# Performance work log

Measured on AMD Instinct MI355X. Metric: run time of the kernel, lower is better.

## Reference

```python
import jax, jax.numpy as jnp
import numpy as np
import math

HEAD = 4

def _neighbors3x3(t):
    # t: [b, g, d, h, w] -> [b, g, d, 9, h, w], zero-padded 3x3 neighborhoods
    b, g, d, h, w = t.shape
    tp = jnp.pad(t, ((0, 0), (0, 0), (0, 0), (1, 1), (1, 1)))
    # torch.nn.Unfold(kernel_size=3) ordering: kernel positions row-major (dy, dx)
    patches = [tp[:, :, :, dy:dy + h, dx:dx + w] for dy in range(3) for dx in range(3)]
    return jnp.stack(patches, axis=3)


def setup_inputs() -> dict:
    key = jax.random.key(0)
    k1, k2 = jax.random.split(key)
    x = jax.random.normal(k1, (8, 128, 96, 96), dtype=jnp.float32)
    # 1x1 conv weight, no bias: [out=3*out_features, in=in_features]
    W_trans = jax.random.normal(k2, (384, 128), dtype=jnp.float32) * 0.05
    return {"x": x, "W_trans": W_trans}


def reference(x, W_trans):
    b, cin, h, w = x.shape
    # 1x1 conv == channel GEMM
    t = jnp.einsum('bchw,oc->bohw', x, W_trans)  # [b, 3*C, h, w]
    q, k, v = jnp.split(t, 3, axis=1)            # each [b, C, h, w]
    C = q.shape[1]
    d = C // HEAD
    q = q.reshape(b, HEAD, d, h, w)
    k = k.reshape(b, HEAD, d, h, w)
    v = v.reshape(b, HEAD, d, h, w)
    kn = _neighbors3x3(k)  # [b, g, d, 9, h, w]
    vn = _neighbors3x3(v)  # [b, g, d, 9, h, w]
    # att[b,g,n,h,w] = <q[b,g,:,h,w], kn[b,g,:,n,h,w]> / sqrt(d)
    att = jnp.einsum('bgdhw,bgdnhw->bgnhw', q, kn) / math.sqrt(d)
    att = jax.nn.softmax(att, axis=2)
    # dropout p=0.4 is identity in eval mode
    out = jnp.einsum('bgnhw,bgdnhw->bgdhw', att, vn)  # [b, g, d, h, w]
    return out.reshape(b, C, h, w)
```

## Files before the change

### kernel.cpp

```cpp
#include <hip/hip_runtime.h>

#define NB     8
#define CIN    128
#define HEADS  4
#define DHEAD  32
#define HDIM   96
#define WDIM   96
#define HW     9216
#define TP     64

typedef __bf16 bf16x8 __attribute__((ext_vector_type(8)));
typedef float  f32x4  __attribute__((ext_vector_type(4)));

__device__ __forceinline__ unsigned f2bf(float f) {
  unsigned u = __float_as_uint(f);
  return (u + 0x7fffu + ((u >> 16) & 1u)) >> 16;
}
__device__ __forceinline__ unsigned pack2(float a, float b) {
  return f2bf(a) | (f2bf(b) << 16);
}
__device__ __forceinline__ float bflo(unsigned u) { return __uint_as_float(u << 16); }
__device__ __forceinline__ float bfhi(unsigned u) { return __uint_as_float(u & 0xffff0000u); }

__global__ __launch_bounds__(256) void wpack_kernel(const float* __restrict__ W,
                                                    uint4* __restrict__ Wf) {
  const int u = blockIdx.x * 256 + threadIdx.x;
  const int lane = u & 63, kb = (u >> 6) & 3, ot = u >> 8;
  const int o = ot * 16 + (lane & 15);
  const int c0 = kb * 32 + (lane >> 4) * 8;
  const float4* w = (const float4*)(W + (size_t)o * CIN + c0);
  float4 w0 = w[0], w1 = w[1];
  uint4 r;
  r.x = pack2(w0.x, w0.y); r.y = pack2(w0.z, w0.w);
  r.z = pack2(w1.x, w1.y); r.w = pack2(w1.z, w1.w);
  Wf[u] = r;
}

__global__ __launch_bounds__(256) void qkv_kernel(const float* __restrict__ x,
                                                  const uint4* __restrict__ Wf,
                                                  unsigned short* __restrict__ qkvb) {
  __shared__ uint4 xs[16 * 64];
  const int b  = blockIdx.y;
  const int p0 = blockIdx.x * TP;
  const int t  = threadIdx.x;

  {
    const int p = t & 63, cg_hi = t >> 6;
    const int pt = p >> 4, n = p & 15;
    const float* xb = x + (size_t)b * CIN * HW + p0 + p;
#pragma unroll
    for (int i = 0; i < 4; ++i) {
      const int cg = i * 4 + cg_hi;
      const int c0 = cg * 8;
      const int kb = cg >> 2, q = cg & 3;
      float f[8];
#pragma unroll
      for (int j = 0; j < 8; ++j) f[j] = xb[(size_t)(c0 + j) * HW];
      uint4 r;
      r.x = pack2(f[0], f[1]); r.y = pack2(f[2], f[3]);
      r.z = pack2(f[4], f[5]); r.w = pack2(f[6], f[7]);
      xs[(pt * 4 + kb) * 64 + q * 16 + n] = r;
    }
  }
  __syncthreads();

  const int wv = t >> 6, lane = t & 63;
  const int colp = lane & 15, quad = lane >> 4;
#pragma unroll 1
  for (int it = 0; it < 6; ++it) {
    const int ot = wv * 6 + it;
    bf16x8 afrag[4];
#pragma unroll
    for (int kb = 0; kb < 4; ++kb) {
      uint4 tmp = Wf[(ot * 4 + kb) * 64 + lane];
      afrag[kb] = *(bf16x8*)&tmp;
    }
    const int o0 = ot * 16 + quad * 4;
    const int which = o0 >> 7, g = (o0 & 127) >> 5, d0 = o0 & 31;
    unsigned short* dst = qkvb
        + (((size_t)(which * NB + b) * HEADS + g) * HW) * DHEAD + d0;
#pragma unroll
    for (int pt = 0; pt < 4; ++pt) {
      f32x4 acc = {0.f, 0.f, 0.f, 0.f};
#pragma unroll
      for (int kb = 0; kb < 4; ++kb) {
        bf16x8 bfrag = *(bf16x8*)&xs[(pt * 4 + kb) * 64 + lane];
        acc = __builtin_amdgcn_mfma_f32_16x16x32_bf16(afrag[kb], bfrag, acc, 0, 0, 0);
      }
      const int pp = p0 + pt * 16 + colp;
      uint2 st;
      st.x = pack2(acc[0], acc[1]);
      st.y = pack2(acc[2], acc[3]);
      *(uint2*)(dst + (size_t)pp * DHEAD) = st;
    }
  }
}

__global__ __launch_bounds__(256) void attn_kernel(const unsigned short* __restrict__ qkvb,
                                                   float* __restrict__ out) {
  const int bg = blockIdx.z;
  const int h  = blockIdx.y * 8 + threadIdx.y;
  const int w  = blockIdx.x * 32 + threadIdx.x;
  const int b  = bg >> 2, g = bg & 3;

  const size_t plane = (size_t)HW * DHEAD;
  const uint4* Qb = (const uint4*)(qkvb + (size_t)bg * plane);
  const uint4* Kb = (const uint4*)(qkvb + (size_t)(32 + bg) * plane);
  const uint4* Vb = (const uint4*)(qkvb + (size_t)(64 + bg) * plane);
  const int p = h * WDIM + w;

  float q[32];
#pragma unroll
  for (int i = 0; i < 4; ++i) {
    uint4 u = Qb[p * 4 + i];
    q[i * 8 + 0] = bflo(u.x); q[i * 8 + 1] = bfhi(u.x);
    q[i * 8 + 2] = bflo(u.y); q[i * 8 + 3] = bfhi(u.y);
    q[i * 8 + 4] = bflo(u.z); q[i * 8 + 5] = bfhi(u.z);
    q[i * 8 + 6] = bflo(u.w); q[i * 8 + 7] = bfhi(u.w);
  }

  float att[9];
#pragma unroll
  for (int nn = 0; nn < 9; ++nn) {
    const int dy = nn / 3 - 1, dx = nn % 3 - 1;
    const int hh = h + dy, ww = w + dx;
    float dot = 0.0f;
    if (hh >= 0 && hh < HDIM && ww >= 0 && ww < WDIM) {
      const int pn = hh * WDIM + ww;
#pragma unroll
      for (int i = 0; i < 4; ++i) {
        uint4 u = Kb[pn * 4 + i];
        dot = fmaf(q[i * 8 + 0], bflo(u.x), dot);
        dot = fmaf(q[i * 8 + 1], bfhi(u.x), dot);
        dot = fmaf(q[i * 8 + 2], bflo(u.y), dot);
        dot = fmaf(q[i * 8 + 3], bfhi(u.y), dot);
        dot = fmaf(q[i * 8 + 4], bflo(u.z), dot);
        dot = fmaf(q[i * 8 + 5], bfhi(u.z), dot);
        dot = fmaf(q[i * 8 + 6], bflo(u.w), dot);
        dot = fmaf(q[i * 8 + 7], bfhi(u.w), dot);
      }
      dot *= 0.17677669529663687f;
    }
    att[nn] = dot;
  }

  float m = att[0];
#pragma unroll
  for (int nn = 1; nn < 9; ++nn) m = fmaxf(m, att[nn]);
  float s = 0.0f;
#pragma unroll
  for (int nn = 0; nn < 9; ++nn) { att[nn] = __expf(att[nn] - m); s += att[nn]; }
  const float inv = 1.0f / s;

  float acc[32];
#pragma unroll
  for (int i = 0; i < 32; ++i) acc[i] = 0.0f;
#pragma unroll
  for (int nn = 0; nn < 9; ++nn) {
    const int dy = nn / 3 - 1, dx = nn % 3 - 1;
    const int hh = h + dy, ww = w + dx;
    if (hh >= 0 && hh < HDIM && ww >= 0 && ww < WDIM) {
      const float wn = att[nn] * inv;
      const int pn = hh * WDIM + ww;
#pragma unroll
      for (int i = 0; i < 4; ++i) {
        uint4 u = Vb[pn * 4 + i];
        acc[i * 8 + 0] = fmaf(wn, bflo(u.x), acc[i * 8 + 0]);
        acc[i * 8 + 1] = fmaf(wn, bfhi(u.x), acc[i * 8 + 1]);
        acc[i * 8 + 2] = fmaf(wn, bflo(u.y), acc[i * 8 + 2]);
        acc[i * 8 + 3] = fmaf(wn, bfhi(u.y), acc[i * 8 + 3]);
        acc[i * 8 + 4] = fmaf(wn, bflo(u.z), acc[i * 8 + 4]);
        acc[i * 8 + 5] = fmaf(wn, bfhi(u.z), acc[i * 8 + 5]);
        acc[i * 8 + 6] = fmaf(wn, bflo(u.w), acc[i * 8 + 6]);
        acc[i * 8 + 7] = fmaf(wn, bfhi(u.w), acc[i * 8 + 7]);
      }
    }
  }

  float* ob = out + ((size_t)b * CIN + (size_t)g * DHEAD) * HW + p;
#pragma unroll
  for (int i = 0; i < 32; ++i) ob[(size_t)i * HW] = acc[i];
}

extern "C" void kernel_launch(void* const* d_in, const int* in_sizes, int n_in,
                              void* d_out, int out_size, void* d_ws, size_t ws_size,
                              hipStream_t stream) {
  (void)in_sizes; (void)n_in; (void)out_size; (void)ws_size;
  const float* x = (const float*)d_in[0];
  const float* W = (const float*)d_in[1];
  float* out = (float*)d_out;

  const size_t qkv_ushorts = (size_t)3 * NB * HEADS * HW * DHEAD;
  unsigned short* qkvb = (unsigned short*)d_ws;
  uint4* Wf = (uint4*)((char*)d_ws + qkv_ushorts * 2);

  wpack_kernel<<<24, 256, 0, stream>>>(W, Wf);
  qkv_kernel<<<dim3(HW / TP, NB), 256, 0, stream>>>(x, Wf, qkvb);
  attn_kernel<<<dim3(WDIM / 32, HDIM / 8, NB * HEADS), dim3(32, 8, 1), 0, stream>>>(qkvb, out);
}
```

Baseline: 127.9 us.

## Stage Q and haloed K/V tiles in shared memory for neighborhood attention

The attention kernel now cooperatively loads the block's Q tile and a zero-padded 10x34 halo of K and V into LDS, then reads the 3x3 neighbors from shared memory. This avoids repeated global/cache reads of each K/V position by up to nine threads and drops the per-neighbor boundary branches. In exchange it uses roughly 60 KB of LDS per block, which limits occupancy, and adds a block-wide barrier before compute.

```diff
diff --git a/kernel.cpp b/kernel.cpp
--- a/kernel.cpp
+++ b/kernel.cpp
@@ -96,52 +96,86 @@
   }
 }
 
+#define KROWS 10
+#define KCOLS 34
+#define KPOS  (KROWS * KCOLS)
+#define QPOS  256
+
 __global__ __launch_bounds__(256) void attn_kernel(const unsigned short* __restrict__ qkvb,
                                                    float* __restrict__ out) {
+  __shared__ uint4 qs[4 * QPOS];
+  __shared__ uint4 ks[4 * KPOS];
+  __shared__ uint4 vs[4 * KPOS];
+
   const int bg = blockIdx.z;
-  const int h  = blockIdx.y * 8 + threadIdx.y;
-  const int w  = blockIdx.x * 32 + threadIdx.x;
+  const int h0 = blockIdx.y * 8;
+  const int w0 = blockIdx.x * 32;
+  const int x  = threadIdx.x, y = threadIdx.y;
+  const int t  = y * 32 + x;
   const int b  = bg >> 2, g = bg & 3;
 
   const size_t plane = (size_t)HW * DHEAD;
-  const uint4* Qb = (const uint4*)(qkvb + (size_t)bg * plane);
-  const uint4* Kb = (const uint4*)(qkvb + (size_t)(32 + bg) * plane);
-  const uint4* Vb = (const uint4*)(qkvb + (size_t)(64 + bg) * plane);
-  const int p = h * WDIM + w;
+  const uint4* Qg = (const uint4*)(qkvb + (size_t)bg * plane);
+  const uint4* Kg = (const uint4*)(qkvb + (size_t)(32 + bg) * plane);
+  const uint4* Vg = (const uint4*)(qkvb + (size_t)(64 + bg) * plane);
+
+  {
+    int u = t;
+#pragma unroll
+    for (int it = 0; it < 4; ++it, u += 256) {
+      const int r = u >> 7, j = u & 127;
+      const int col = j >> 2, c = j & 3;
+      const int p = (h0 + r) * WDIM + w0 + col;
+      qs[c * QPOS + r * 32 + col] = Qg[(size_t)p * 4 + c];
+    }
+  }
+  for (int u = t; u < KPOS * 4; u += 256) {
+    const int r = u / 136;
+    const int j = u - r * 136;
+    const int cc = j >> 2, c = j & 3;
+    const int hh = h0 - 1 + r, ww = w0 - 1 + cc;
+    uint4 kk = {0u, 0u, 0u, 0u}, vv = {0u, 0u, 0u, 0u};
+    if (hh >= 0 && hh < HDIM && ww >= 0 && ww < WDIM) {
+      const size_t p = (size_t)(hh * WDIM + ww) * 4 + c;
+      kk = Kg[p];
+      vv = Vg[p];
+    }
+    const int dst = c * KPOS + r * KCOLS + cc;
+    ks[dst] = kk;
+    vs[dst] = vv;
+  }
+  __syncthreads();
 
   float q[32];
 #pragma unroll
-  for (int i = 0; i < 4; ++i) {
-    uint4 u = Qb[p * 4 + i];
-    q[i * 8 + 0] = bflo(u.x); q[i * 8 + 1] = bfhi(u.x);
-    q[i * 8 + 2] = bflo(u.y); q[i * 8 + 3] = bfhi(u.y);
-    q[i * 8 + 4] = bflo(u.z); q[i * 8 + 5] = bfhi(u.z);
-    q[i * 8 + 6] = bflo(u.w); q[i * 8 + 7] = bfhi(u.w);
-  }
+  for (int c = 0; c < 4; ++c) {
+    uint4 u = qs[c * QPOS + t];
+    q[c * 8 + 0] = bflo(u.x); q[c * 8 + 1] = bfhi(u.x);
+    q[c * 8 + 2] = bflo(u.y); q[c * 8 + 3] = bfhi(u.y);
+    q[c * 8 + 4] = bflo(u.z); q[c * 8 + 5] = bfhi(u.z);
+    q[c * 8 + 6] = bflo(u.w); q[c * 8 + 7] = bfhi(u.w);
+  }
+
+  const int pbase = (y + 1) * KCOLS + (x + 1);
 
   float att[9];
 #pragma unroll
   for (int nn = 0; nn < 9; ++nn) {
-    const int dy = nn / 3 - 1, dx = nn % 3 - 1;
-    const int hh = h + dy, ww = w + dx;
+    const int pn = pbase + (nn / 3 - 1) * KCOLS + (nn % 3 - 1);
     float dot = 0.0f;
-    if (hh >= 0 && hh < HDIM && ww >= 0 && ww < WDIM) {
-      const int pn = hh * WDIM + ww;
-#pragma unroll
-      for (int i = 0; i < 4; ++i) {
-        uint4 u = Kb[pn * 4 + i];
-        dot = fmaf(q[i * 8 + 0], bflo(u.x), dot);
-        dot = fmaf(q[i * 8 + 1], bfhi(u.x), dot);
-        dot = fmaf(q[i * 8 + 2], bflo(u.y), dot);
-        dot = fmaf(q[i * 8 + 3], bfhi(u.y), dot);
-        dot = fmaf(q[i * 8 + 4], bflo(u.z), dot);
-        dot = fmaf(q[i * 8 + 5], bfhi(u.z), dot);
-        dot = fmaf(q[i * 8 + 6], bflo(u.w), dot);
-        dot = fmaf(q[i * 8 + 7], bfhi(u.w), dot);
-      }
-      dot *= 0.17677669529663687f;
-    }
-    att[nn] = dot;
+#pragma unroll
+    for (int c = 0; c < 4; ++c) {
+      uint4 u = ks[c * KPOS + pn];
+      dot = fmaf(q[c * 8 + 0], bflo(u.x), dot);
+      dot = fmaf(q[c * 8 + 1], bfhi(u.x), dot);
+      dot = fmaf(q[c * 8 + 2], bflo(u.y), dot);
+      dot = fmaf(q[c * 8 + 3], bfhi(u.y), dot);
+      dot = fmaf(q[c * 8 + 4], bflo(u.z), dot);
+      dot = fmaf(q[c * 8 + 5], bfhi(u.z), dot);
+      dot = fmaf(q[c * 8 + 6], bflo(u.w), dot);
+      dot = fmaf(q[c * 8 + 7], bfhi(u.w), dot);
+    }
+    att[nn] = dot * 0.17677669529663687f;
   }
 
   float m = att[0];
@@ -157,26 +191,23 @@
   for (int i = 0; i < 32; ++i) acc[i] = 0.0f;
 #pragma unroll
   for (int nn = 0; nn < 9; ++nn) {
-    const int dy = nn / 3 - 1, dx = nn % 3 - 1;
-    const int hh = h + dy, ww = w + dx;
-    if (hh >= 0 && hh < HDIM && ww >= 0 && ww < WDIM) {
-      const float wn = att[nn] * inv;
-      const int pn = hh * WDIM + ww;
-#pragma unroll
-      for (int i = 0; i < 4; ++i) {
-        uint4 u = Vb[pn * 4 + i];
-        acc[i * 8 + 0] = fmaf(wn, bflo(u.x), acc[i * 8 + 0]);
-        acc[i * 8 + 1] = fmaf(wn, bfhi(u.x), acc[i * 8 + 1]);
-        acc[i * 8 + 2] = fmaf(wn, bflo(u.y), acc[i * 8 + 2]);
-        acc[i * 8 + 3] = fmaf(wn, bfhi(u.y), acc[i * 8 + 3]);
-        acc[i * 8 + 4] = fmaf(wn, bflo(u.z), acc[i * 8 + 4]);
-        acc[i * 8 + 5] = fmaf(wn, bfhi(u.z), acc[i * 8 + 5]);
-        acc[i * 8 + 6] = fmaf(wn, bflo(u.w), acc[i * 8 + 6]);
-        acc[i * 8 + 7] = fmaf(wn, bfhi(u.w), acc[i * 8 + 7]);
-      }
-    }
-  }
-
+    const float wn = att[nn] * inv;
+    const int pn = pbase + (nn / 3 - 1) * KCOLS + (nn % 3 - 1);
+#pragma unroll
+    for (int c = 0; c < 4; ++c) {
+      uint4 u = vs[c * KPOS + pn];
+      acc[c * 8 + 0] = fmaf(wn, bflo(u.x), acc[c * 8 + 0]);
+      acc[c * 8 + 1] = fmaf(wn, bfhi(u.x), acc[c * 8 + 1]);
+      acc[c * 8 + 2] = fmaf(wn, bflo(u.y), acc[c * 8 + 2]);
+      acc[c * 8 + 3] = fmaf(wn, bfhi(u.y), acc[c * 8 + 3]);
+      acc[c * 8 + 4] = fmaf(wn, bflo(u.z), acc[c * 8 + 4]);
+      acc[c * 8 + 5] = fmaf(wn, bfhi(u.z), acc[c * 8 + 5]);
+      acc[c * 8 + 6] = fmaf(wn, bflo(u.w), acc[c * 8 + 6]);
+      acc[c * 8 + 7] = fmaf(wn, bfhi(u.w), acc[c * 8 + 7]);
+    }
+  }
+
+  const int p = (h0 + y) * WDIM + (w0 + x);
   float* ob = out + ((size_t)b * CIN + (size_t)g * DHEAD) * HW + p;
 #pragma unroll
   for (int i = 0; i < 32; ++i) ob[(size_t)i * HW] = acc[i];
```

Result: faster. 124.7 us (-2.5%).
